# Performance work log

Measured on AMD Instinct MI355X. Metric: run time of the kernel, lower is better.

Reference implementation:

```python
import jax, jax.numpy as jnp
import numpy as np
from jax import lax

T = 4096
IN_CH = 1024   # per-embedding channels; LSTM input = 2*IN_CH
HID = 2048     # embedding_size == hidden_dim


def setup_inputs() -> dict:
    key = jax.random.key(0)
    ks = jax.random.split(key, 6)
    s = 1.0 / np.sqrt(HID)  # torch LSTMCell init scale
    return {
        "src_embedding": jax.random.normal(ks[0], (T, IN_CH), jnp.float32),
        "dst_embedding": jax.random.normal(ks[1], (T, IN_CH), jnp.float32),
        "W_ih": jax.random.uniform(ks[2], (4 * HID, 2 * IN_CH), jnp.float32, -s, s),
        "W_hh": jax.random.uniform(ks[3], (4 * HID, HID), jnp.float32, -s, s),
        "b_ih": jax.random.uniform(ks[4], (4 * HID,), jnp.float32, -s, s),
        "b_hh": jax.random.uniform(ks[5], (4 * HID,), jnp.float32, -s, s),
    }


def reference(src_embedding, dst_embedding, W_ih, W_hh, b_ih, b_hh):
    # inp: [T, 2*IN_CH]; sequential batch-1 LSTMCell over T steps (PyTorch gate order i,f,g,o)
    x = jnp.concatenate((src_embedding, dst_embedding), axis=1)
    H = W_hh.shape[1]
    b = b_ih + b_hh  # [4H]
    # Precompute the input projection for all timesteps in one big GEMM.
    xg = x @ W_ih.T + b  # [T, 4H]
    h0 = jnp.zeros((H,), x.dtype)
    c0 = jnp.zeros((H,), x.dtype)

    def step(carry, xg_t):
        h, c = carry
        gates = xg_t + h @ W_hh.T  # [4H]
        i, f, g, o = jnp.split(gates, 4)
        i = jax.nn.sigmoid(i)
        f = jax.nn.sigmoid(f)
        g = jnp.tanh(g)
        o = jax.nn.sigmoid(o)
        c_new = f * c + i * g
        h_new = o * jnp.tanh(c_new)
        return (h_new, c_new), None

    (h, c), _ = lax.scan(step, (h0, c0), xg)
    return h.reshape(1, -1)  # matches module's returned self.h of shape [1, H]
```

## Files before the change

kernel.cpp:

```cpp
#include <hip/hip_runtime.h>
#include <hip/hip_bf16.h>


#define T_STEPS 4096
#define FOURH   8192

typedef _Float16 f16;
typedef _Float16 f16x2 __attribute__((ext_vector_type(2)));
typedef _Float16 f16x8 __attribute__((ext_vector_type(8)));
typedef float    f32x4 __attribute__((ext_vector_type(4)));

#if __has_builtin(__builtin_amdgcn_fdot2)
#define FDOT2(a, b, c) __builtin_amdgcn_fdot2((a), (b), (c), false)
#else
#define FDOT2(a, b, c) ((c) + (float)(a)[0] * (float)(b)[0] + (float)(a)[1] * (float)(b)[1])
#endif

__global__ void init_tags(unsigned long long* __restrict__ hbuf) {
    int i = blockIdx.x * 256 + threadIdx.x;
    if (i < 2048) hbuf[i] = (i < 1024) ? (1ULL << 32) : 0ULL;
}

#define GBM 128
#define GBN 128
#define GBK 32
#define LDT 40

__global__ __launch_bounds__(256) void xg_gemm(
    const float* __restrict__ src, const float* __restrict__ dst,
    const float* __restrict__ Wih, const float* __restrict__ bi,
    const float* __restrict__ bh, f16* __restrict__ xg) {
    __shared__ __align__(16) f16 As[GBM * LDT];
    __shared__ __align__(16) f16 Bs[GBN * LDT];

    const int tid = threadIdx.x;
    const int bx  = blockIdx.x;
    const int tm  = bx >> 6, tn = bx & 63;
    const int m0  = tm * GBM, n0 = tn * GBN;
    const int lane = tid & 63, wv = tid >> 6;
    const int wm = (wv >> 1) * 64, wn = (wv & 1) * 64;
    const int fr = lane & 15, kg = lane >> 4;

    const int srow = tid >> 1;
    const int sk   = (tid & 1) * 16;

    f32x4 acc[4][4];
#pragma unroll
    for (int i = 0; i < 4; ++i)
#pragma unroll
        for (int j = 0; j < 4; ++j) acc[i][j] = (f32x4){0.f, 0.f, 0.f, 0.f};

    for (int kt = 0; kt < 2048 / GBK; ++kt) {
        const int gk = kt * GBK + sk;
        {
            const float* ap = (gk < 1024) ? (src + (size_t)(m0 + srow) * 1024 + gk)
                                          : (dst + (size_t)(m0 + srow) * 1024 + (gk - 1024));
            float4 fa = *(const float4*)(ap + 0);
            float4 fb = *(const float4*)(ap + 4);
            float4 fc = *(const float4*)(ap + 8);
            float4 fd = *(const float4*)(ap + 12);
            f16x8 lo, hi;
            lo[0] = (f16)fa.x; lo[1] = (f16)fa.y; lo[2] = (f16)fa.z; lo[3] = (f16)fa.w;
            lo[4] = (f16)fb.x; lo[5] = (f16)fb.y; lo[6] = (f16)fb.z; lo[7] = (f16)fb.w;
            hi[0] = (f16)fc.x; hi[1] = (f16)fc.y; hi[2] = (f16)fc.z; hi[3] = (f16)fc.w;
            hi[4] = (f16)fd.x; hi[5] = (f16)fd.y; hi[6] = (f16)fd.z; hi[7] = (f16)fd.w;
            *(f16x8*)&As[srow * LDT + sk]     = lo;
            *(f16x8*)&As[srow * LDT + sk + 8] = hi;
        }
        {
            const float* bp = Wih + (size_t)(n0 + srow) * 2048 + gk;
            float4 fa = *(const float4*)(bp + 0);
            float4 fb = *(const float4*)(bp + 4);
            float4 fc = *(const float4*)(bp + 8);
            float4 fd = *(const float4*)(bp + 12);
            f16x8 lo, hi;
            lo[0] = (f16)fa.x; lo[1] = (f16)fa.y; lo[2] = (f16)fa.z; lo[3] = (f16)fa.w;
            lo[4] = (f16)fb.x; lo[5] = (f16)fb.y; lo[6] = (f16)fb.z; lo[7] = (f16)fb.w;
            hi[0] = (f16)fc.x; hi[1] = (f16)fc.y; hi[2] = (f16)fc.z; hi[3] = (f16)fc.w;
            hi[4] = (f16)fd.x; hi[5] = (f16)fd.y; hi[6] = (f16)fd.z; hi[7] = (f16)fd.w;
            *(f16x8*)&Bs[srow * LDT + sk]     = lo;
            *(f16x8*)&Bs[srow * LDT + sk + 8] = hi;
        }
        __syncthreads();
        f16x8 a[4], b[4];
#pragma unroll
        for (int m = 0; m < 4; ++m) a[m] = *(const f16x8*)&As[(wm + m * 16 + fr) * LDT + kg * 8];
#pragma unroll
        for (int n = 0; n < 4; ++n) b[n] = *(const f16x8*)&Bs[(wn + n * 16 + fr) * LDT + kg * 8];
#pragma unroll
        for (int m = 0; m < 4; ++m)
#pragma unroll
            for (int n = 0; n < 4; ++n)
                acc[m][n] = __builtin_amdgcn_mfma_f32_16x16x32_f16(a[m], b[n], acc[m][n], 0, 0, 0);
        __syncthreads();
    }
#pragma unroll
    for (int n = 0; n < 4; ++n) {
        const int col = n0 + wn + n * 16 + fr;
        const float bias = bi[col] + bh[col];
#pragma unroll
        for (int m = 0; m < 4; ++m) {
            const int rb = m0 + wm + m * 16 + kg * 4;
#pragma unroll
            for (int r = 0; r < 4; ++r)
                xg[(size_t)(rb + r) * FOURH + col] = (f16)(acc[m][n][r] + bias);
        }
    }
}

__global__ __launch_bounds__(256, 1) void lstm_scan(
    const float* __restrict__ Whh, const f16* __restrict__ xg,
    unsigned long long* __restrict__ hbuf, float* __restrict__ out) {
    const int w    = blockIdx.x;
    const int tid  = threadIdx.x;
    const int lane = tid & 63;
    const int gt   = tid >> 6;
    const int m0   = w * 8;

    __shared__ unsigned h2s[1024];
    __shared__ float scratch[4][8][68];
    __shared__ float gatebuf[4][8];

    f16x2 wreg[8][16];
#pragma unroll
    for (int r = 0; r < 8; ++r) {
        const float* wrow = Whh + (size_t)(gt * 2048 + m0 + r) * 2048;
#pragma unroll
        for (int j = 0; j < 16; ++j) {
            const int p = lane + 64 * j;
            float2 f = *(const float2*)(wrow + 2 * p);
            f16x2 v; v[0] = (f16)f.x; v[1] = (f16)f.y;
            wreg[r][j] = v;
        }
    }

    unsigned long long* base0 = hbuf;
    unsigned long long* base1 = hbuf + 1024;
    float c_st = 0.f;
    const int p0 = gt * 256 + lane;

    for (int t = 0; t < T_STEPS; ++t) {
        float xgv = 0.f;
        if ((lane & 7) == 0)
            xgv = (float)xg[(size_t)t * FOURH + gt * 2048 + m0 + (lane >> 3)];

        unsigned long long* cur = (t & 1) ? base1 : base0;
        const unsigned tagw = (unsigned)(t + 1);
        unsigned long long v0, v1, v2, v3;
        for (;;) {
            v0 = __hip_atomic_load(cur + p0,       __ATOMIC_RELAXED, __HIP_MEMORY_SCOPE_AGENT);
            v1 = __hip_atomic_load(cur + p0 + 64,  __ATOMIC_RELAXED, __HIP_MEMORY_SCOPE_AGENT);
            v2 = __hip_atomic_load(cur + p0 + 128, __ATOMIC_RELAXED, __HIP_MEMORY_SCOPE_AGENT);
            v3 = __hip_atomic_load(cur + p0 + 192, __ATOMIC_RELAXED, __HIP_MEMORY_SCOPE_AGENT);
            if ((unsigned)(v0 >> 32) >= tagw && (unsigned)(v1 >> 32) >= tagw &&
                (unsigned)(v2 >> 32) >= tagw && (unsigned)(v3 >> 32) >= tagw)
                break;
            __builtin_amdgcn_s_sleep(1);
        }
        h2s[p0]       = (unsigned)v0;
        h2s[p0 + 64]  = (unsigned)v1;
        h2s[p0 + 128] = (unsigned)v2;
        h2s[p0 + 192] = (unsigned)v3;
        __syncthreads();

        f16x2 hreg[16];
#pragma unroll
        for (int j = 0; j < 16; ++j)
            hreg[j] = __builtin_bit_cast(f16x2, h2s[lane + 64 * j]);
        float accv[8];
#pragma unroll
        for (int r = 0; r < 8; ++r) {
            float a = 0.f;
#pragma unroll
            for (int j = 0; j < 16; ++j) a = FDOT2(wreg[r][j], hreg[j], a);
            accv[r] = a;
        }
#pragma unroll
        for (int r = 0; r < 8; ++r) scratch[gt][r][lane] = accv[r];
        __syncthreads();
        {
            const int r = lane >> 3, cc = lane & 7;
            const float* s = &scratch[gt][r][cc * 8];
            float s0 = s[0] + s[1] + s[2] + s[3] + s[4] + s[5] + s[6] + s[7];
            s0 += __shfl_xor(s0, 1);
            s0 += __shfl_xor(s0, 2);
            s0 += __shfl_xor(s0, 4);
            if (cc == 0) gatebuf[gt][r] = s0 + xgv;
        }
        __syncthreads();

        if (gt == 0) {
            float hval = 0.f;
            if (lane < 8) {
                const int m = lane;
                float gi = gatebuf[0][m], gf = gatebuf[1][m];
                float gg = gatebuf[2][m], go = gatebuf[3][m];
                float ig = 1.f / (1.f + __expf(-gi));
                float fg = 1.f / (1.f + __expf(-gf));
                float g  = 1.f - 2.f / (__expf(2.f * gg) + 1.f);
                float og = 1.f / (1.f + __expf(-go));
                float c  = fg * c_st + ig * g;
                c_st = c;
                hval = og * (1.f - 2.f / (__expf(2.f * c) + 1.f));
                if (t == T_STEPS - 1) out[m0 + m] = hval;
            }
            if (t != T_STEPS - 1) {
                float hlo = __shfl(hval, 2 * (lane & 3));
                float hhi = __shfl(hval, 2 * (lane & 3) + 1);
                if (lane < 4) {
                    f16x2 hp; hp[0] = (f16)hlo; hp[1] = (f16)hhi;
                    unsigned long long val = ((unsigned long long)(unsigned)(t + 2) << 32) |
                                             (unsigned long long)__builtin_bit_cast(unsigned, hp);
                    unsigned long long* nxt = (t & 1) ? base0 : base1;
                    __hip_atomic_store(nxt + w * 4 + lane, val,
                                       __ATOMIC_RELAXED, __HIP_MEMORY_SCOPE_AGENT);
                }
            }
        }
    }
}

extern "C" void kernel_launch(void* const* d_in, const int* in_sizes, int n_in,
                              void* d_out, int out_size, void* d_ws, size_t ws_size,
                              hipStream_t stream) {
    const float* src = (const float*)d_in[0];
    const float* dst = (const float*)d_in[1];
    const float* Wih = (const float*)d_in[2];
    const float* Whh = (const float*)d_in[3];
    const float* bi  = (const float*)d_in[4];
    const float* bh  = (const float*)d_in[5];
    float* out = (float*)d_out;

    f16* xg = (f16*)d_ws;
    unsigned long long* hbuf =
        (unsigned long long*)((char*)d_ws + ((size_t)64 << 20));

    hipLaunchKernelGGL(init_tags, dim3(8), dim3(256), 0, stream, hbuf);
    hipLaunchKernelGGL(xg_gemm, dim3((4096 / GBM) * (FOURH / GBN)), dim3(256), 0, stream,
                       src, dst, Wih, bi, bh, xg);
    hipLaunchKernelGGL(lstm_scan, dim3(256), dim3(256), 0, stream, Whh, xg, hbuf, out);
}
```

Measured before the change: 10.29 ms.

## Split recurrent matvec by K across waves, cutting per-step barriers to one

Measured after the change: 8.957 ms. 1.15x faster.

```diff
diff --git a/kernel.cpp b/kernel.cpp
--- a/kernel.cpp
+++ b/kernel.cpp
@@ -114,110 +114,120 @@
     const int w    = blockIdx.x;
     const int tid  = threadIdx.x;
     const int lane = tid & 63;
-    const int gt   = tid >> 6;
-    const int m0   = w * 8;
-
-    __shared__ unsigned h2s[1024];
-    __shared__ float scratch[4][8][68];
-    __shared__ float gatebuf[4][8];
-
-    f16x2 wreg[8][16];
-#pragma unroll
-    for (int r = 0; r < 8; ++r) {
-        const float* wrow = Whh + (size_t)(gt * 2048 + m0 + r) * 2048;
-#pragma unroll
-        for (int j = 0; j < 16; ++j) {
-            const int p = lane + 64 * j;
-            float2 f = *(const float2*)(wrow + 2 * p);
-            f16x2 v; v[0] = (f16)f.x; v[1] = (f16)f.y;
-            wreg[r][j] = v;
-        }
-    }
-
-    unsigned long long* base0 = hbuf;
-    unsigned long long* base1 = hbuf + 1024;
+    const int wv   = tid >> 6;
+
+    __shared__ float scratch[2][4][32][64];
+
+    const int k0 = 512 * wv + 8 * lane;
+    unsigned wreg[32][4];
+#pragma unroll
+    for (int r = 0; r < 32; ++r) {
+        const size_t row = (size_t)((r & 3) * 2048 + w * 8 + (r >> 2));
+        const float4* wp = (const float4*)(Whh + row * 2048 + k0);
+        float4 a = wp[0], b = wp[1];
+        f16x2 p0; p0[0] = (f16)a.x; p0[1] = (f16)a.y;
+        f16x2 p1; p1[0] = (f16)a.z; p1[1] = (f16)a.w;
+        f16x2 p2; p2[0] = (f16)b.x; p2[1] = (f16)b.y;
+        f16x2 p3; p3[0] = (f16)b.z; p3[1] = (f16)b.w;
+        wreg[r][0] = __builtin_bit_cast(unsigned, p0);
+        wreg[r][1] = __builtin_bit_cast(unsigned, p1);
+        wreg[r][2] = __builtin_bit_cast(unsigned, p2);
+        wreg[r][3] = __builtin_bit_cast(unsigned, p3);
+    }
+#pragma unroll
+    for (int r = 0; r < 32; ++r)
+#pragma unroll
+        for (int i = 0; i < 4; ++i)
+            asm volatile("" : "+v"(wreg[r][i]));
+
+    unsigned long long* bb0 = hbuf;
+    unsigned long long* bb1 = hbuf + 1024;
+    const int e0 = 256 * wv + 4 * lane;
+
+    const int q     = tid & 7;
+    const int rR    = tid >> 3;
+    const int vR    = q >> 1, halfR = q & 1;
+    const int swzR  = ((rR & 7) << 2) ^ (vR << 3);
+    const int xcol  = (rR & 3) * 2048 + w * 8 + (rR >> 2);
+    const int wswz  = ((0) << 2);
+
     float c_st = 0.f;
-    const int p0 = gt * 256 + lane;
 
     for (int t = 0; t < T_STEPS; ++t) {
         float xgv = 0.f;
-        if ((lane & 7) == 0)
-            xgv = (float)xg[(size_t)t * FOURH + gt * 2048 + m0 + (lane >> 3)];
-
-        unsigned long long* cur = (t & 1) ? base1 : base0;
+        if (q == 0) xgv = (float)xg[(size_t)t * FOURH + xcol];
+
+        unsigned long long* cur = (t & 1) ? bb1 : bb0;
         const unsigned tagw = (unsigned)(t + 1);
-        unsigned long long v0, v1, v2, v3;
+        unsigned long long p0, p1, p2, p3;
         for (;;) {
-            v0 = __hip_atomic_load(cur + p0,       __ATOMIC_RELAXED, __HIP_MEMORY_SCOPE_AGENT);
-            v1 = __hip_atomic_load(cur + p0 + 64,  __ATOMIC_RELAXED, __HIP_MEMORY_SCOPE_AGENT);
-            v2 = __hip_atomic_load(cur + p0 + 128, __ATOMIC_RELAXED, __HIP_MEMORY_SCOPE_AGENT);
-            v3 = __hip_atomic_load(cur + p0 + 192, __ATOMIC_RELAXED, __HIP_MEMORY_SCOPE_AGENT);
-            if ((unsigned)(v0 >> 32) >= tagw && (unsigned)(v1 >> 32) >= tagw &&
-                (unsigned)(v2 >> 32) >= tagw && (unsigned)(v3 >> 32) >= tagw)
+            p0 = __hip_atomic_load(cur + e0 + 0, __ATOMIC_RELAXED, __HIP_MEMORY_SCOPE_AGENT);
+            p1 = __hip_atomic_load(cur + e0 + 1, __ATOMIC_RELAXED, __HIP_MEMORY_SCOPE_AGENT);
+            p2 = __hip_atomic_load(cur + e0 + 2, __ATOMIC_RELAXED, __HIP_MEMORY_SCOPE_AGENT);
+            p3 = __hip_atomic_load(cur + e0 + 3, __ATOMIC_RELAXED, __HIP_MEMORY_SCOPE_AGENT);
+            if ((unsigned)(p0 >> 32) >= tagw && (unsigned)(p1 >> 32) >= tagw &&
+                (unsigned)(p2 >> 32) >= tagw && (unsigned)(p3 >> 32) >= tagw)
                 break;
             __builtin_amdgcn_s_sleep(1);
         }
-        h2s[p0]       = (unsigned)v0;
-        h2s[p0 + 64]  = (unsigned)v1;
-        h2s[p0 + 128] = (unsigned)v2;
-        h2s[p0 + 192] = (unsigned)v3;
+        f16x2 h0 = __builtin_bit_cast(f16x2, (unsigned)p0);
+        f16x2 h1 = __builtin_bit_cast(f16x2, (unsigned)p1);
+        f16x2 h2 = __builtin_bit_cast(f16x2, (unsigned)p2);
+        f16x2 h3 = __builtin_bit_cast(f16x2, (unsigned)p3);
+
+        float* sc = &scratch[t & 1][wv][0][0];
+#pragma unroll
+        for (int r = 0; r < 32; ++r) {
+            float a = FDOT2(__builtin_bit_cast(f16x2, wreg[r][0]), h0, 0.f);
+            a = FDOT2(__builtin_bit_cast(f16x2, wreg[r][1]), h1, a);
+            a = FDOT2(__builtin_bit_cast(f16x2, wreg[r][2]), h2, a);
+            a = FDOT2(__builtin_bit_cast(f16x2, wreg[r][3]), h3, a);
+            sc[r * 64 + (lane ^ (((r & 7) << 2) ^ (wv << 3)))] = a;
+        }
         __syncthreads();
 
-        f16x2 hreg[16];
-#pragma unroll
-        for (int j = 0; j < 16; ++j)
-            hreg[j] = __builtin_bit_cast(f16x2, h2s[lane + 64 * j]);
-        float accv[8];
-#pragma unroll
-        for (int r = 0; r < 8; ++r) {
-            float a = 0.f;
-#pragma unroll
-            for (int j = 0; j < 16; ++j) a = FDOT2(wreg[r][j], hreg[j], a);
-            accv[r] = a;
-        }
-#pragma unroll
-        for (int r = 0; r < 8; ++r) scratch[gt][r][lane] = accv[r];
-        __syncthreads();
-        {
-            const int r = lane >> 3, cc = lane & 7;
-            const float* s = &scratch[gt][r][cc * 8];
-            float s0 = s[0] + s[1] + s[2] + s[3] + s[4] + s[5] + s[6] + s[7];
-            s0 += __shfl_xor(s0, 1);
-            s0 += __shfl_xor(s0, 2);
-            s0 += __shfl_xor(s0, 4);
-            if (cc == 0) gatebuf[gt][r] = s0 + xgv;
-        }
-        __syncthreads();
-
-        if (gt == 0) {
-            float hval = 0.f;
-            if (lane < 8) {
-                const int m = lane;
-                float gi = gatebuf[0][m], gf = gatebuf[1][m];
-                float gg = gatebuf[2][m], go = gatebuf[3][m];
-                float ig = 1.f / (1.f + __expf(-gi));
-                float fg = 1.f / (1.f + __expf(-gf));
-                float g  = 1.f - 2.f / (__expf(2.f * gg) + 1.f);
-                float og = 1.f / (1.f + __expf(-go));
-                float c  = fg * c_st + ig * g;
-                c_st = c;
-                hval = og * (1.f - 2.f / (__expf(2.f * c) + 1.f));
-                if (t == T_STEPS - 1) out[m0 + m] = hval;
+        const float* sr = &scratch[t & 1][vR][rR][0];
+        float s0 = 0.f;
+#pragma unroll
+        for (int kk = 0; kk < 8; ++kk) {
+            const int idx = ((halfR << 5) + (kk << 2)) ^ swzR;
+            f32x4 vv = *(const f32x4*)&sr[idx];
+            s0 += vv[0] + vv[1] + vv[2] + vv[3];
+        }
+        s0 += __shfl_xor(s0, 1);
+        s0 += __shfl_xor(s0, 2);
+        s0 += __shfl_xor(s0, 4);
+        s0 += xgv;
+
+        const int base = lane & 32;
+        float gi = __shfl(s0, base + 0);
+        float gf = __shfl(s0, base + 8);
+        float gg = __shfl(s0, base + 16);
+        float go = __shfl(s0, base + 24);
+        float ig = 1.f / (1.f + __expf(-gi));
+        float fg = 1.f / (1.f + __expf(-gf));
+        float g  = 1.f - 2.f / (__expf(2.f * gg) + 1.f);
+        float og = 1.f / (1.f + __expf(-go));
+        float c  = fg * c_st + ig * g;
+        c_st = c;
+        float h = og * (1.f - 2.f / (__expf(2.f * c) + 1.f));
+
+        if (t == T_STEPS - 1) {
+            if ((lane & 31) == 0) out[w * 8 + 2 * wv + (lane >> 5)] = h;
+        } else {
+            float hh = __shfl(h, 32);
+            if (lane == 0) {
+                f16x2 hp; hp[0] = (f16)h; hp[1] = (f16)hh;
+                unsigned long long val =
+                    ((unsigned long long)(unsigned)(t + 2) << 32) |
+                    (unsigned long long)__builtin_bit_cast(unsigned, hp);
+                unsigned long long* nxt = (t & 1) ? bb0 : bb1;
+                __hip_atomic_store(nxt + (w * 4 + wv), val,
+                                   __ATOMIC_RELAXED, __HIP_MEMORY_SCOPE_AGENT);
             }
-            if (t != T_STEPS - 1) {
-                float hlo = __shfl(hval, 2 * (lane & 3));
-                float hhi = __shfl(hval, 2 * (lane & 3) + 1);
-                if (lane < 4) {
-                    f16x2 hp; hp[0] = (f16)hlo; hp[1] = (f16)hhi;
-                    unsigned long long val = ((unsigned long long)(unsigned)(t + 2) << 32) |
-                                             (unsigned long long)__builtin_bit_cast(unsigned, hp);
-                    unsigned long long* nxt = (t & 1) ? base0 : base1;
-                    __hip_atomic_store(nxt + w * 4 + lane, val,
-                                       __ATOMIC_RELAXED, __HIP_MEMORY_SCOPE_AGENT);
-                }
-            }
-        }
-    }
+        }
+    }
+    (void)wswz;
 }
 
 extern "C" void kernel_launch(void* const* d_in, const int* in_sizes, int n_in,
```
